# Performance work log

Measured on AMD Instinct MI355X. Metric: run time of the kernel, lower is better.

Reference implementation:

```python
import jax, jax.numpy as jnp
import numpy as np

SLOPE = (1.0 / 8 + 1.0 / 3) / 2  # F.rrelu in eval mode: mean of (lower, upper)
DILS = [1, 2, 4, 8, 16]
WINDOW = 32
TEMP = 0.1


def rrelu(x):
    return jnp.where(x >= 0, x, x * SLOPE)


def conv1d(x, w, b, dil):
    # x: [B, Cin, T], w: [Cout, Cin, K]
    y = jax.lax.conv_general_dilated(x, w, window_strides=(1,), padding='VALID',
                                     rhs_dilation=(dil,),
                                     dimension_numbers=('NCH', 'OIH', 'NCH'))
    return y + b[None, :, None]


def setup_inputs() -> dict:
    key = jax.random.key(0)
    ks = jax.random.split(key, 32)
    B, T, R, K, W = 16, 16384, 8, 2, WINDOW
    ins = [1, 64, 64, 64, 64]
    outs = [64, 64, 64, 64, R]
    inp = {"x": jax.random.normal(ks[0], (B, 1, T), jnp.float32)}
    for l in range(5):
        inp[f"cw{l}"] = jax.random.normal(ks[1 + l], (outs[l], ins[l], K), jnp.float32) * 0.1
        inp[f"cb{l}"] = jax.random.normal(ks[6 + l], (outs[l],), jnp.float32) * 0.1
    pc = [(2 * R, 2 * R), (2 * R, 2 * R), (1, 2 * R)]  # params_convs, kernel 1
    for i, (o, ci) in enumerate(pc):
        inp[f"mw{i}"] = jax.random.normal(ks[11 + i], (o, ci, 1), jnp.float32) * 0.1
        inp[f"mb{i}"] = jax.random.normal(ks[14 + i], (o,), jnp.float32) * 0.1
    inp["sqrt_cov_tt"] = jax.random.uniform(ks[17], (R, 1), jnp.float32)
    inp["fish_jt"] = jax.random.normal(ks[18], (R, W), jnp.float32) * 0.01
    u = jax.random.uniform(ks[19], (B, T, R), jnp.float32, minval=1e-6, maxval=1.0 - 1e-6)
    inp["gumbel"] = -jnp.log(-jnp.log(u))
    return inp


def reference(x, cw0, cb0, cw1, cb1, cw2, cb2, cw3, cb3, cw4, cb4,
              mw0, mb0, mw1, mb1, mw2, mb2, sqrt_cov_tt, fish_jt, gumbel):
    pad = sum(DILS)
    T = x.shape[-1]
    W = WINDOW
    # forward_pass: causal dilated conv stack with rrelu
    h = jnp.pad(x, ((0, 0), (0, 0), (pad, 0)))
    for w, b, d in zip([cw0, cw1, cw2, cw3, cw4], [cb0, cb1, cb2, cb3, cb4], DILS):
        h = rrelu(conv1d(h, w, b, d))
    # h: [B, R, T]
    logits = jnp.transpose(h, (0, 2, 1))  # [B, T, R]
    gen_z = jax.nn.softmax((logits + gumbel) / TEMP, axis=-1)
    gen_z = jnp.transpose(gen_z, (0, 2, 1))  # [B, R, T]
    # params_convs (1x1 convs): conv -> (rrelu, conv) x2
    m = conv1d(jnp.concatenate([gen_z, h], axis=1), mw0, mb0, 1)
    m = conv1d(rrelu(m), mw1, mb1, 1)
    mus = conv1d(rrelu(m), mw2, mb2, 1)  # [B, 1, T]
    cov_tt = jnp.einsum('brt,rl->blt', gen_z, sqrt_cov_tt) ** 2  # [B, 1, T]
    cov_tt = cov_tt[:, :, W:T]  # [B, 1, T-W]
    fj = jnp.einsum('brt,rw->bwt', gen_z, fish_jt)[:, :, W:T]  # [B, W, T-W]
    # vectorized sliding window: x_window[b, j, t] = x[b, 0, t + j]
    idx = jnp.arange(W)[:, None] + jnp.arange(T - W)[None, :]  # [W, T-W]
    xw = x[:, 0, :][:, idx]   # [B, W, T-W]
    mw_ = mus[:, 0, :][:, idx]  # [B, W, T-W]
    _mus = mus[:, 0, W:T] - jnp.einsum('bwt,bwt->bt', cov_tt * fj, xw - mw_)
    return (_mus, gen_z)
```

## Files before the change

kernel.cpp:

```cpp
#include <hip/hip_runtime.h>
#include <hip/hip_bf16.h>

#define NT 1024
#define TT 192
#define PBA 222
#define PBB 220
#define NB 16
#define T_ 16384
#define W_ 32
#define TW_ (T_ - W_)
#define SLOPE_C 0.22916666666666666f

#define WIMG_W4   49152
#define WIMG_CST  53248
#define WIMG_USH  55296

typedef short v8s __attribute__((ext_vector_type(8)));
typedef float v4f __attribute__((ext_vector_type(4)));

__device__ __forceinline__ float rr(float v){ return v >= 0.f ? v : v * SLOPE_C; }
__device__ __forceinline__ ushort f2bs(float f){ __hip_bfloat16 h = __float2bfloat16(f); return *(ushort*)&h; }
__device__ __forceinline__ float bs2f(ushort u){ union{unsigned i; float f;} v; v.i = ((unsigned)u) << 16; return v.f; }

__device__ __forceinline__ int agr(int p, int gi){ return p*128 + ((gi ^ (p & 15)) << 3); }
__device__ __forceinline__ int widx(int wr, int ci){
  return wr*64 + ((((ci >> 3) ^ (wr & 7)) << 3) | (ci & 7));
}

__global__ __launch_bounds__(256) void kW(
    const float* __restrict__ cw1, const float* __restrict__ cw2,
    const float* __restrict__ cw3, const float* __restrict__ cw4,
    const float* __restrict__ cw0, const float* __restrict__ cb0,
    const float* __restrict__ cb1, const float* __restrict__ cb2,
    const float* __restrict__ cb3, const float* __restrict__ cb4,
    const float* __restrict__ mw0, const float* __restrict__ mb0,
    const float* __restrict__ mw1, const float* __restrict__ mb1,
    const float* __restrict__ mw2, const float* __restrict__ mb2,
    ushort* __restrict__ wimg)
{
  const int id = blockIdx.x*256 + threadIdx.x;
  if (id < 24576){
    int l = id >> 13, e = id & 8191;
    const float* src = (l == 0) ? cw1 : ((l == 1) ? cw2 : cw3);
    int c = e >> 7, rem = e & 127, ci = rem >> 1, k = rem & 1;
    float v = src[e];
    ushort h = f2bs(v), lo = f2bs(v - bs2f(h));
    int ix = widx(k*64 + c, ci);
    wimg[l*16384 + ix] = h;
    wimg[l*16384 + 8192 + ix] = lo;
  } else if (id < 25600){
    int e = id - 24576;
    int c = e >> 7, rem = e & 127, ci = rem >> 1, k = rem & 1;
    float v = cw4[e];
    ushort h = f2bs(v), lo = f2bs(v - bs2f(h));
    int ix = widx(k*16 + c, ci);
    wimg[WIMG_W4 + ix] = h;
    wimg[WIMG_W4 + 2048 + ix] = lo;
  } else if (id < 27648){
    int e = id - 25600;
    int pl = e >> 10, rem = e & 1023, k = rem >> 9, r2 = rem & 511;
    int m = 8 + (r2 >> 6), ci = r2 & 63;
    wimg[WIMG_W4 + pl*2048 + widx(k*16 + m, ci)] = 0;
  } else if (id < 28672){
    int e = id - 27648;
    float v = 0.f;
    if      (e < 256) v = mw0[e];
    else if (e < 512) v = mw1[e - 256];
    else if (e < 528) v = mw2[e - 512];
    else if (e < 544) v = mb0[e - 528];
    else if (e < 560) v = mb1[e - 544];
    else if (e < 561) v = mb2[0];
    else if (e >= 576 && e < 584) v = cb4[e - 576];
    else if (e >= 592 && e < 720) v = cw0[e - 592];
    else if (e >= 720 && e < 784) v = cb0[e - 720];
    else if (e >= 784 && e < 848) v = cb1[e - 784];
    else if (e >= 848 && e < 912) v = cb2[e - 848];
    else if (e >= 912 && e < 976) v = cb3[e - 912];
    ((float*)(wimg + WIMG_CST))[e] = v;
  }
}

template<int D, int NSRC, int NDST>
__device__ __forceinline__ void mfma_layer(const ushort* __restrict__ src,
    ushort* __restrict__ dst, const ushort* __restrict__ wlds,
    const float* __restrict__ cbias, int tid)
{
  const int wave = tid >> 6;
  if (wave >= 7) return;
  const int lane = tid & 63;
  const int n = lane & 15, quad = lane >> 4;
  const int p0 = wave * 32;

  v4f acc[8];
  const v4f vz = {0.f, 0.f, 0.f, 0.f};
#pragma unroll
  for (int i = 0; i < 8; ++i) acc[i] = vz;

#pragma unroll
  for (int tap = 0; tap < 2; ++tap){
#pragma unroll
    for (int kb = 0; kb < 2; ++kb){
      const int kg = kb*4 + quad;
      v8s wh[4], wl[4], ah[2], al[2];
#pragma unroll
      for (int mt = 0; mt < 4; ++mt){
        int wr = tap*64 + mt*16 + n;
        int base = wr*64 + ((kg ^ (wr & 7)) << 3);
        wh[mt] = *(const v8s*)(wlds + base);
        wl[mt] = *(const v8s*)(wlds + 8192 + base);
      }
#pragma unroll
      for (int nt = 0; nt < 2; ++nt){
        int p = p0 + nt*16 + n + tap*D;
        if (p >= NSRC) p = NSRC - 1;
        ah[nt] = *(const v8s*)(src + agr(p, kg));
        al[nt] = *(const v8s*)(src + agr(p, 8 + kg));
      }
#pragma unroll
      for (int nt = 0; nt < 2; ++nt)
#pragma unroll
        for (int mt = 0; mt < 4; ++mt){
          v4f a = acc[nt*4 + mt];
          a = __builtin_amdgcn_mfma_f32_16x16x32_bf16(wh[mt], ah[nt], a, 0, 0, 0);
          a = __builtin_amdgcn_mfma_f32_16x16x32_bf16(wh[mt], al[nt], a, 0, 0, 0);
          a = __builtin_amdgcn_mfma_f32_16x16x32_bf16(wl[mt], ah[nt], a, 0, 0, 0);
          acc[nt*4 + mt] = a;
        }
    }
  }

#pragma unroll
  for (int nt = 0; nt < 2; ++nt){
    int p = p0 + nt*16 + n;
    if (p < NDST){
#pragma unroll
      for (int mt = 0; mt < 4; ++mt){
#pragma unroll
        for (int r = 0; r < 4; r += 2){
          int c = mt*16 + quad*4 + r;
          float y0 = rr(acc[nt*4 + mt][r]     + cbias[c]);
          float y1 = rr(acc[nt*4 + mt][r + 1] + cbias[c + 1]);
          ushort h0 = f2bs(y0), h1 = f2bs(y1);
          ushort l0 = f2bs(y0 - bs2f(h0)), l1 = f2bs(y1 - bs2f(h1));
          int gh = agr(p, c >> 3)       + (c & 7);
          int gl = agr(p, 8 + (c >> 3)) + (c & 7);
          *(unsigned*)(dst + gh) = (unsigned)h0 | ((unsigned)h1 << 16);
          *(unsigned*)(dst + gl) = (unsigned)l0 | ((unsigned)l1 << 16);
        }
      }
    }
  }
}

template<bool GZT>
__global__ __launch_bounds__(NT, 4) void kA(
    const float* __restrict__ x, const float* __restrict__ gum,
    const ushort* __restrict__ wimg,
    float* __restrict__ ws_mus, float* __restrict__ out_gz,
    float* __restrict__ gzt)
{
  __shared__ __align__(16) ushort bufA[PBA*128];
  __shared__ __align__(16) ushort bufB[PBB*128];
  __shared__ __align__(16) ushort wlds[16384];
  __shared__ __align__(16) ushort w4lds[4096];
  __shared__ __align__(16) float  cstl[1024];

  float* xbuf = (float*)bufB;

  const int tile = blockIdx.x, b = blockIdx.y;
  const int t0 = tile * TT;
  const int core = (T_ - t0 < TT) ? (T_ - t0) : TT;
  const int tid = threadIdx.x;

  const int nx = core + 31;
  for (int i = tid; i < nx; i += NT){
    int g = t0 + i;
    xbuf[i] = (g >= 31) ? x[(size_t)b*T_ + g - 31] : 0.f;
  }
  for (int i = tid; i < 2048; i += NT)
    *(v8s*)(wlds + i*8) = *(const v8s*)(wimg + i*8);
  for (int i = tid; i < 512; i += NT)
    *(v8s*)(w4lds + i*8) = *(const v8s*)(wimg + WIMG_W4 + i*8);
  for (int i = tid; i < 512; i += NT)
    ((float2*)cstl)[i] = ((const float2*)(wimg + WIMG_CST))[i];
  __syncthreads();

  {
    const int n0 = core + 30;
    for (int i = tid; i < PBA*64; i += NT){
      int p = i >> 6, c = i & 63;
      float y = 0.f;
      if (p < n0) y = rr(cstl[720 + c] + cstl[592 + 2*c]*xbuf[p] + cstl[593 + 2*c]*xbuf[p + 1]);
      ushort h = f2bs(y); ushort lo = f2bs(y - bs2f(h));
      bufA[agr(p, c >> 3)       + (c & 7)] = h;
      bufA[agr(p, 8 + (c >> 3)) + (c & 7)] = lo;
    }
  }
  __syncthreads();

  mfma_layer<2, PBA, PBB>(bufA, bufB, wlds, cstl + 784, tid);
  __syncthreads();
  for (int i = tid; i < 2048; i += NT)
    *(v8s*)(wlds + i*8) = *(const v8s*)(wimg + 16384 + i*8);
  __syncthreads();
  mfma_layer<4, PBB, PBA>(bufB, bufA, wlds, cstl + 848, tid);
  __syncthreads();
  for (int i = tid; i < 2048; i += NT)
    *(v8s*)(wlds + i*8) = *(const v8s*)(wimg + 32768 + i*8);
  __syncthreads();
  mfma_layer<8, PBA, PBB>(bufA, bufB, wlds, cstl + 912, tid);
  __syncthreads();

  float* h4s = (float*)bufA;
  {
    const int wave = tid >> 6;
    if (wave < 7){
      const int lane = tid & 63;
      const int n = lane & 15, quad = lane >> 4;
      const int p0 = wave * 32;
      v4f acc2[2];
      const v4f vz = {0.f, 0.f, 0.f, 0.f};
      acc2[0] = vz; acc2[1] = vz;
#pragma unroll
      for (int tap = 0; tap < 2; ++tap){
#pragma unroll
        for (int kb = 0; kb < 2; ++kb){
          const int kg = kb*4 + quad;
          int wr = tap*16 + n;
          int base = wr*64 + ((kg ^ (wr & 7)) << 3);
          v8s wh = *(const v8s*)(w4lds + base);
          v8s wl = *(const v8s*)(w4lds + 2048 + base);
#pragma unroll
          for (int nt = 0; nt < 2; ++nt){
            int p = p0 + nt*16 + n + tap*16;
            if (p >= PBB) p = PBB - 1;
            v8s ah = *(const v8s*)(bufB + agr(p, kg));
            v8s al = *(const v8s*)(bufB + agr(p, 8 + kg));
            v4f a = acc2[nt];
            a = __builtin_amdgcn_mfma_f32_16x16x32_bf16(wh, ah, a, 0, 0, 0);
            a = __builtin_amdgcn_mfma_f32_16x16x32_bf16(wh, al, a, 0, 0, 0);
            a = __builtin_amdgcn_mfma_f32_16x16x32_bf16(wl, ah, a, 0, 0, 0);
            acc2[nt] = a;
          }
        }
      }
#pragma unroll
      for (int nt = 0; nt < 2; ++nt){
        int p = p0 + nt*16 + n;
        if (p < core && quad < 2){
#pragma unroll
          for (int r = 0; r < 4; ++r){
            int c = quad*4 + r;
            h4s[c*TT + p] = rr(acc2[nt][r] + cstl[576 + c]);
          }
        }
      }
    }
  }
  __syncthreads();

  if (tid < core){
    const int t = t0 + tid;
    float l[8];
#pragma unroll
    for (int r = 0; r < 8; ++r) l[r] = h4s[r*TT + tid];
    float gv[8];
    *(float4*)&gv[0] = *(const float4*)(gum + (size_t)(b*T_ + t)*8);
    *(float4*)&gv[4] = *(const float4*)(gum + (size_t)(b*T_ + t)*8 + 4);
    float s[8], mx = -1e30f;
#pragma unroll
    for (int r = 0; r < 8; ++r){ s[r] = (l[r] + gv[r]) * 10.0f; mx = fmaxf(mx, s[r]); }
    float e[8], sum = 0.f;
#pragma unroll
    for (int r = 0; r < 8; ++r){ e[r] = __expf(s[r] - mx); sum += e[r]; }
    float inv = 1.0f / sum;
    float z[8];
#pragma unroll
    for (int r = 0; r < 8; ++r){
      z[r] = e[r] * inv;
      out_gz[(size_t)(b*8 + r)*T_ + t] = z[r];
    }
    if (GZT){
      *(float4*)(gzt + (size_t)(b*T_ + t)*8)     = make_float4(z[0], z[1], z[2], z[3]);
      *(float4*)(gzt + (size_t)(b*T_ + t)*8 + 4) = make_float4(z[4], z[5], z[6], z[7]);
    }
    float m0[16];
#pragma unroll
    for (int o = 0; o < 16; ++o){
      float a = cstl[528 + o];
#pragma unroll
      for (int i = 0; i < 8; ++i) a += cstl[o*16 + i] * z[i];
#pragma unroll
      for (int i = 0; i < 8; ++i) a += cstl[o*16 + 8 + i] * l[i];
      m0[o] = rr(a);
    }
    float m1[16];
#pragma unroll
    for (int o = 0; o < 16; ++o){
      float a = cstl[544 + o];
#pragma unroll
      for (int i = 0; i < 16; ++i) a += cstl[256 + o*16 + i] * m0[i];
      m1[o] = rr(a);
    }
    float mu = cstl[560];
#pragma unroll
    for (int i = 0; i < 16; ++i) mu += cstl[512 + i] * m1[i];
    ws_mus[(size_t)b*T_ + t] = mu;
  }
}

template<bool GZT>
__global__ __launch_bounds__(256) void kB(
    const float* __restrict__ x, const float* __restrict__ fish,
    const float* __restrict__ sct, const float* __restrict__ ws_mus,
    const float* __restrict__ gz, float* __restrict__ out0)
{
  __shared__ float xm[288], mm[288], fs[256], sc[8];
  const int b = blockIdx.y;
  const int s = blockIdx.x * 256;
  const int tid = threadIdx.x;
  for (int i = tid; i < 288; i += 256){
    int g = s + i;
    bool ok = g < T_;
    xm[i] = ok ? x[(size_t)b*T_ + g] : 0.f;
    mm[i] = ok ? ws_mus[(size_t)b*T_ + g] : 0.f;
  }
  fs[tid] = fish[tid];
  if (tid < 8) sc[tid] = sct[tid];
  __syncthreads();
  const int tp = s + tid;
  if (tp < TW_){
    const int t = W_ + tp;
    float z[8];
    if (GZT){
      *(float4*)&z[0] = *(const float4*)(gz + (size_t)(b*T_ + t)*8);
      *(float4*)&z[4] = *(const float4*)(gz + (size_t)(b*T_ + t)*8 + 4);
    } else {
#pragma unroll
      for (int r = 0; r < 8; ++r) z[r] = gz[(size_t)(b*8 + r)*T_ + t];
    }
    float cv = 0.f;
#pragma unroll
    for (int r = 0; r < 8; ++r) cv += sc[r] * z[r];
    cv *= cv;
    float acc = 0.f;
#pragma unroll 4
    for (int w = 0; w < 32; ++w){
      float fj = 0.f;
#pragma unroll
      for (int r = 0; r < 8; ++r) fj += z[r] * fs[r*32 + w];
      acc += fj * (xm[tid + w] - mm[tid + w]);
    }
    out0[(size_t)b*TW_ + tp] = mm[tid + 32] - cv * acc;
  }
}

extern "C" void kernel_launch(void* const* d_in, const int* in_sizes, int n_in,
                              void* d_out, int out_size, void* d_ws, size_t ws_size,
                              hipStream_t stream)
{
  const float* x   = (const float*)d_in[0];
  const float* cw0 = (const float*)d_in[1];
  const float* cb0 = (const float*)d_in[2];
  const float* cw1 = (const float*)d_in[3];
  const float* cb1 = (const float*)d_in[4];
  const float* cw2 = (const float*)d_in[5];
  const float* cb2 = (const float*)d_in[6];
  const float* cw3 = (const float*)d_in[7];
  const float* cb3 = (const float*)d_in[8];
  const float* cw4 = (const float*)d_in[9];
  const float* cb4 = (const float*)d_in[10];
  const float* mw0 = (const float*)d_in[11];
  const float* mb0 = (const float*)d_in[12];
  const float* mw1 = (const float*)d_in[13];
  const float* mb1 = (const float*)d_in[14];
  const float* mw2 = (const float*)d_in[15];
  const float* mb2 = (const float*)d_in[16];
  const float* sct = (const float*)d_in[17];
  const float* fish= (const float*)d_in[18];
  const float* gum = (const float*)d_in[19];

  float* out0   = (float*)d_out;
  float* out_gz = out0 + NB*TW_;
  float* ws_mus = (float*)d_ws;
  ushort* wimg  = (ushort*)(ws_mus + (size_t)NB*T_);
  float* gzt    = ws_mus + (size_t)NB*T_ + WIMG_USH/2;

  const size_t need_gzt = ((size_t)NB*T_ + WIMG_USH/2 + (size_t)8*NB*T_) * sizeof(float);
  const bool use_t = ws_size >= need_gzt;

  kW<<<112, 256, 0, stream>>>(cw1, cw2, cw3, cw4, cw0, cb0, cb1, cb2, cb3, cb4,
                              mw0, mb0, mw1, mb1, mw2, mb2, wimg);

  dim3 gA((T_ + TT - 1) / TT, NB);
  dim3 gB((TW_ + 255) / 256, NB);
  if (use_t){
    kA<true><<<gA, NT, 0, stream>>>(x, gum, wimg, ws_mus, out_gz, gzt);
    kB<true><<<gB, 256, 0, stream>>>(x, fish, sct, ws_mus, gzt, out0);
  } else {
    kA<false><<<gA, NT, 0, stream>>>(x, gum, wimg, ws_mus, out_gz, gzt);
    kB<false><<<gB, 256, 0, stream>>>(x, fish, sct, ws_mus, out_gz, out0);
  }
}
```

Measured before the change: 231.3 us.

## Fuse window-reduction kernel into conv kernel with overlapping tiles

Merges the separate sliding-window kernel into the main conv/softmax kernel. Tiles now overlap by 32 timesteps (160 outputs per 192 computed) so mus and gen_z for each window stay in shared memory, with gen_z held as bf16. This removes the workspace round trip for mus and gen_z and one kernel launch. In exchange it recomputes about 20% of the conv stack, rounds gen_z to bf16 in the window reduction, and changes block size from 1024 to 512 threads.

```diff
diff --git a/kernel.cpp b/kernel.cpp
--- a/kernel.cpp
+++ b/kernel.cpp
@@ -1,8 +1,10 @@
 #include <hip/hip_runtime.h>
 #include <hip/hip_bf16.h>
 
-#define NT 1024
-#define TT 192
+#define NT 512
+#define TS 160
+#define TC 192
+#define NTILE 103
 #define PBA 222
 #define PBB 220
 #define NB 16
@@ -13,7 +15,7 @@
 
 #define WIMG_W4   49152
 #define WIMG_CST  53248
-#define WIMG_USH  55296
+#define WIMG_USH  56320
 
 typedef short v8s __attribute__((ext_vector_type(8)));
 typedef float v4f __attribute__((ext_vector_type(4)));
@@ -36,6 +38,7 @@
     const float* __restrict__ mw0, const float* __restrict__ mb0,
     const float* __restrict__ mw1, const float* __restrict__ mb1,
     const float* __restrict__ mw2, const float* __restrict__ mb2,
+    const float* __restrict__ fish, const float* __restrict__ sct,
     ushort* __restrict__ wimg)
 {
   const int id = blockIdx.x*256 + threadIdx.x;
@@ -61,21 +64,23 @@
     int pl = e >> 10, rem = e & 1023, k = rem >> 9, r2 = rem & 511;
     int m = 8 + (r2 >> 6), ci = r2 & 63;
     wimg[WIMG_W4 + pl*2048 + widx(k*16 + m, ci)] = 0;
-  } else if (id < 28672){
+  } else if (id < 29184){
     int e = id - 27648;
     float v = 0.f;
-    if      (e < 256) v = mw0[e];
-    else if (e < 512) v = mw1[e - 256];
-    else if (e < 528) v = mw2[e - 512];
-    else if (e < 544) v = mb0[e - 528];
-    else if (e < 560) v = mb1[e - 544];
-    else if (e < 561) v = mb2[0];
-    else if (e >= 576 && e < 584) v = cb4[e - 576];
-    else if (e >= 592 && e < 720) v = cw0[e - 592];
-    else if (e >= 720 && e < 784) v = cb0[e - 720];
-    else if (e >= 784 && e < 848) v = cb1[e - 784];
-    else if (e >= 848 && e < 912) v = cb2[e - 848];
-    else if (e >= 912 && e < 976) v = cb3[e - 912];
+    if      (e < 256)  v = mw0[e];
+    else if (e < 512)  v = mw1[e - 256];
+    else if (e < 528)  v = mw2[e - 512];
+    else if (e < 544)  v = mb0[e - 528];
+    else if (e < 560)  v = mb1[e - 544];
+    else if (e < 561)  v = mb2[0];
+    else if (e >= 576 && e < 584)  v = cb4[e - 576];
+    else if (e >= 592 && e < 720)  v = cw0[e - 592];
+    else if (e >= 720 && e < 784)  v = cb0[e - 720];
+    else if (e >= 784 && e < 848)  v = cb1[e - 784];
+    else if (e >= 848 && e < 912)  v = cb2[e - 848];
+    else if (e >= 912 && e < 976)  v = cb3[e - 912];
+    else if (e >= 1024 && e < 1280) v = fish[e - 1024];
+    else if (e >= 1280 && e < 1288) v = sct[e - 1280];
     ((float*)(wimg + WIMG_CST))[e] = v;
   }
 }
@@ -152,48 +157,58 @@
   }
 }
 
-template<bool GZT>
-__global__ __launch_bounds__(NT, 4) void kA(
+__global__ __launch_bounds__(NT) void kAB(
     const float* __restrict__ x, const float* __restrict__ gum,
     const ushort* __restrict__ wimg,
-    float* __restrict__ ws_mus, float* __restrict__ out_gz,
-    float* __restrict__ gzt)
+    float* __restrict__ out0, float* __restrict__ out_gz)
 {
   __shared__ __align__(16) ushort bufA[PBA*128];
   __shared__ __align__(16) ushort bufB[PBB*128];
   __shared__ __align__(16) ushort wlds[16384];
   __shared__ __align__(16) ushort w4lds[4096];
-  __shared__ __align__(16) float  cstl[1024];
+  __shared__ __align__(16) float  cstl[1536];
 
   float* xbuf = (float*)bufB;
+  float*  fA   = (float*)bufA;
+  float*  h4s  = fA;
+  float*  musl = fA + 1536;
+  float*  pacc = fA + 1728;
+  float*  xg   = fA + 2240;
+  ushort* zl   = (ushort*)(fA + 2464);
 
   const int tile = blockIdx.x, b = blockIdx.y;
-  const int t0 = tile * TT;
-  const int core = (T_ - t0 < TT) ? (T_ - t0) : TT;
+  const int o0 = tile * TS;
+  const int core = (T_ - o0 < TC) ? (T_ - o0) : TC;
+  const int ncut = (TW_ - o0 < TS) ? (TW_ - o0) : TS;
   const int tid = threadIdx.x;
 
   const int nx = core + 31;
   for (int i = tid; i < nx; i += NT){
-    int g = t0 + i;
+    int g = o0 + i;
     xbuf[i] = (g >= 31) ? x[(size_t)b*T_ + g - 31] : 0.f;
   }
   for (int i = tid; i < 2048; i += NT)
     *(v8s*)(wlds + i*8) = *(const v8s*)(wimg + i*8);
   for (int i = tid; i < 512; i += NT)
     *(v8s*)(w4lds + i*8) = *(const v8s*)(wimg + WIMG_W4 + i*8);
-  for (int i = tid; i < 512; i += NT)
+  for (int i = tid; i < 768; i += NT)
     ((float2*)cstl)[i] = ((const float2*)(wimg + WIMG_CST))[i];
   __syncthreads();
 
   {
     const int n0 = core + 30;
-    for (int i = tid; i < PBA*64; i += NT){
-      int p = i >> 6, c = i & 63;
-      float y = 0.f;
-      if (p < n0) y = rr(cstl[720 + c] + cstl[592 + 2*c]*xbuf[p] + cstl[593 + 2*c]*xbuf[p + 1]);
-      ushort h = f2bs(y); ushort lo = f2bs(y - bs2f(h));
-      bufA[agr(p, c >> 3)       + (c & 7)] = h;
-      bufA[agr(p, 8 + (c >> 3)) + (c & 7)] = lo;
+    for (int i = tid; i < PBA*32; i += NT){
+      int p = i >> 5, c = (i & 31)*2;
+      float y0 = 0.f, y1 = 0.f;
+      if (p < n0){
+        float xp = xbuf[p], xq = xbuf[p + 1];
+        y0 = rr(cstl[720 + c]     + cstl[592 + 2*c]*xp     + cstl[593 + 2*c]*xq);
+        y1 = rr(cstl[720 + c + 1] + cstl[594 + 2*c]*xp     + cstl[595 + 2*c]*xq);
+      }
+      ushort h0 = f2bs(y0), h1 = f2bs(y1);
+      ushort l0 = f2bs(y0 - bs2f(h0)), l1 = f2bs(y1 - bs2f(h1));
+      *(unsigned*)(bufA + agr(p, c >> 3)       + (c & 7)) = (unsigned)h0 | ((unsigned)h1 << 16);
+      *(unsigned*)(bufA + agr(p, 8 + (c >> 3)) + (c & 7)) = (unsigned)l0 | ((unsigned)l1 << 16);
     }
   }
   __syncthreads();
@@ -211,7 +226,6 @@
   mfma_layer<8, PBA, PBB>(bufA, bufB, wlds, cstl + 912, tid);
   __syncthreads();
 
-  float* h4s = (float*)bufA;
   {
     const int wave = tid >> 6;
     if (wave < 7){
@@ -251,7 +265,7 @@
 #pragma unroll
           for (int r = 0; r < 4; ++r){
             int c = quad*4 + r;
-            h4s[c*TT + p] = rr(acc2[nt][r] + cstl[576 + c]);
+            h4s[c*TC + p] = rr(acc2[nt][r] + cstl[576 + c]);
           }
         }
       }
@@ -260,10 +274,10 @@
   __syncthreads();
 
   if (tid < core){
-    const int t = t0 + tid;
+    const int j = tid, t = o0 + j;
     float l[8];
 #pragma unroll
-    for (int r = 0; r < 8; ++r) l[r] = h4s[r*TT + tid];
+    for (int r = 0; r < 8; ++r) l[r] = h4s[r*TC + j];
     float gv[8];
     *(float4*)&gv[0] = *(const float4*)(gum + (size_t)(b*T_ + t)*8);
     *(float4*)&gv[4] = *(const float4*)(gum + (size_t)(b*T_ + t)*8 + 4);
@@ -280,10 +294,9 @@
       z[r] = e[r] * inv;
       out_gz[(size_t)(b*8 + r)*T_ + t] = z[r];
     }
-    if (GZT){
-      *(float4*)(gzt + (size_t)(b*T_ + t)*8)     = make_float4(z[0], z[1], z[2], z[3]);
-      *(float4*)(gzt + (size_t)(b*T_ + t)*8 + 4) = make_float4(z[4], z[5], z[6], z[7]);
-    }
+#pragma unroll
+    for (int r = 0; r < 8; r += 2)
+      *(unsigned*)(zl + j*8 + r) = (unsigned)f2bs(z[r]) | ((unsigned)f2bs(z[r+1]) << 16);
     float m0[16];
 #pragma unroll
     for (int o = 0; o < 16; ++o){
@@ -305,53 +318,47 @@
     float mu = cstl[560];
 #pragma unroll
     for (int i = 0; i < 16; ++i) mu += cstl[512 + i] * m1[i];
-    ws_mus[(size_t)b*T_ + t] = mu;
-  }
-}
-
-template<bool GZT>
-__global__ __launch_bounds__(256) void kB(
-    const float* __restrict__ x, const float* __restrict__ fish,
-    const float* __restrict__ sct, const float* __restrict__ ws_mus,
-    const float* __restrict__ gz, float* __restrict__ out0)
-{
-  __shared__ float xm[288], mm[288], fs[256], sc[8];
-  const int b = blockIdx.y;
-  const int s = blockIdx.x * 256;
-  const int tid = threadIdx.x;
-  for (int i = tid; i < 288; i += 256){
-    int g = s + i;
-    bool ok = g < T_;
-    xm[i] = ok ? x[(size_t)b*T_ + g] : 0.f;
-    mm[i] = ok ? ws_mus[(size_t)b*T_ + g] : 0.f;
-  }
-  fs[tid] = fish[tid];
-  if (tid < 8) sc[tid] = sct[tid];
-  __syncthreads();
-  const int tp = s + tid;
-  if (tp < TW_){
-    const int t = W_ + tp;
+    musl[j] = mu;
+  } else if (tid >= 256 && tid < 480){
+    int k = tid - 256;
+    int g = o0 + k;
+    xg[k] = (g < T_) ? x[(size_t)b*T_ + g] : 0.f;
+  }
+  __syncthreads();
+
+  {
+    const int h = tid >> 8, i = tid & 255;
+    if (i < ncut){
+      float z[8];
+      v8s zv = *(const v8s*)(zl + (i + 32)*8);
+#pragma unroll
+      for (int r = 0; r < 8; ++r) z[r] = bs2f((ushort)zv[r]);
+      float acc = 0.f;
+      const int w0 = h*16;
+#pragma unroll
+      for (int w = 0; w < 16; ++w){
+        float fj = 0.f;
+#pragma unroll
+        for (int r = 0; r < 8; ++r) fj += z[r] * cstl[1024 + r*32 + w0 + w];
+        acc += fj * (xg[i + w0 + w] - musl[i + w0 + w]);
+      }
+      pacc[h*256 + i] = acc;
+    }
+  }
+  __syncthreads();
+
+  if (tid < ncut){
+    const int i = tid;
     float z[8];
-    if (GZT){
-      *(float4*)&z[0] = *(const float4*)(gz + (size_t)(b*T_ + t)*8);
-      *(float4*)&z[4] = *(const float4*)(gz + (size_t)(b*T_ + t)*8 + 4);
-    } else {
-#pragma unroll
-      for (int r = 0; r < 8; ++r) z[r] = gz[(size_t)(b*8 + r)*T_ + t];
-    }
+    v8s zv = *(const v8s*)(zl + (i + 32)*8);
+#pragma unroll
+    for (int r = 0; r < 8; ++r) z[r] = bs2f((ushort)zv[r]);
     float cv = 0.f;
 #pragma unroll
-    for (int r = 0; r < 8; ++r) cv += sc[r] * z[r];
+    for (int r = 0; r < 8; ++r) cv += cstl[1280 + r] * z[r];
     cv *= cv;
-    float acc = 0.f;
-#pragma unroll 4
-    for (int w = 0; w < 32; ++w){
-      float fj = 0.f;
-#pragma unroll
-      for (int r = 0; r < 8; ++r) fj += z[r] * fs[r*32 + w];
-      acc += fj * (xm[tid + w] - mm[tid + w]);
-    }
-    out0[(size_t)b*TW_ + tp] = mm[tid + 32] - cv * acc;
+    float acc = pacc[i] + pacc[256 + i];
+    out0[(size_t)b*TW_ + o0 + i] = musl[i + 32] - cv * acc;
   }
 }
 
@@ -382,23 +389,11 @@
 
   float* out0   = (float*)d_out;
   float* out_gz = out0 + NB*TW_;
-  float* ws_mus = (float*)d_ws;
-  ushort* wimg  = (ushort*)(ws_mus + (size_t)NB*T_);
-  float* gzt    = ws_mus + (size_t)NB*T_ + WIMG_USH/2;
-
-  const size_t need_gzt = ((size_t)NB*T_ + WIMG_USH/2 + (size_t)8*NB*T_) * sizeof(float);
-  const bool use_t = ws_size >= need_gzt;
-
-  kW<<<112, 256, 0, stream>>>(cw1, cw2, cw3, cw4, cw0, cb0, cb1, cb2, cb3, cb4,
-                              mw0, mb0, mw1, mb1, mw2, mb2, wimg);
-
-  dim3 gA((T_ + TT - 1) / TT, NB);
-  dim3 gB((TW_ + 255) / 256, NB);
-  if (use_t){
-    kA<true><<<gA, NT, 0, stream>>>(x, gum, wimg, ws_mus, out_gz, gzt);
-    kB<true><<<gB, 256, 0, stream>>>(x, fish, sct, ws_mus, gzt, out0);
-  } else {
-    kA<false><<<gA, NT, 0, stream>>>(x, gum, wimg, ws_mus, out_gz, gzt);
-    kB<false><<<gB, 256, 0, stream>>>(x, fish, sct, ws_mus, out_gz, out0);
-  }
-}
+  ushort* wimg  = (ushort*)d_ws;
+
+  kW<<<114, 256, 0, stream>>>(cw1, cw2, cw3, cw4, cw0, cb0, cb1, cb2, cb3, cb4,
+                              mw0, mb0, mw1, mb1, mw2, mb2, fish, sct, wimg);
+
+  dim3 gA(NTILE, NB);
+  kAB<<<gA, NT, 0, stream>>>(x, gum, wimg, out0, out_gz);
+}
```

New measurement: 249.7 us. +7.9%, slower.
